# Performance work log

Measured on AMD Instinct MI355X. Metric: run time of the kernel, lower is better.

Reference implementation:

```python
import jax, jax.numpy as jnp
import numpy as np

LMAX = 6
F_IN = 512      # sphere_fdim
F_HID = 8       # f_hidden
N_PTS = 192     # s2 healpix grid points (projector & feature-sphere kernel)
N_SO3GRID = 4000  # SO3Activation grid (resolution=10, ~20x10x20)
N_CONVGRID = 192  # so3_near_identity_grid (8 alpha x 3 beta x 8 gamma)
S2_DIM = (LMAX + 1) ** 2                            # 49
SO3_DIM = sum((2 * l + 1) ** 2 for l in range(LMAX + 1))  # 455
B = 128
C_ENC = 2048
H = W = 7


def setup_inputs() -> dict:
    key = jax.random.key(0)
    ks = jax.random.split(key, 11)
    return {
        "fmap": jax.random.normal(ks[0], (B, C_ENC, H, W), jnp.float32),
        "conv_w": jax.random.normal(ks[1], (F_IN, C_ENC), jnp.float32) / np.sqrt(C_ENC).astype(np.float32),
        "conv_b": jnp.zeros((F_IN,), jnp.float32),
        "proj_w": jax.random.uniform(ks[2], (H, W, N_PTS), jnp.float32) / (H * W),
        "proj_Y": jax.random.normal(ks[3], (N_PTS, S2_DIM), jnp.float32),
        "fs_w": jax.random.normal(ks[4], (F_IN, F_HID, N_PTS), jnp.float32),
        "fs_Y": jax.random.normal(ks[5], (N_PTS, S2_DIM), jnp.float32),
        "act_to": jax.random.normal(ks[6], (SO3_DIM, N_SO3GRID), jnp.float32) / np.sqrt(SO3_DIM).astype(np.float32),
        "act_from": jax.random.normal(ks[7], (N_SO3GRID, SO3_DIM), jnp.float32) / np.float32(N_SO3GRID),
        "so3_w": jax.random.normal(ks[8], (F_HID, 1, N_CONVGRID), jnp.float32),
        "so3_D": jax.random.normal(ks[9], (N_CONVGRID, SO3_DIM), jnp.float32),
    }


def _s2_to_so3_linear(x, psi, f_in):
    # e3nn o3.Linear(s2_irreps -> so3_irreps, internal_weights=False).
    # x: (B, f_in, S2_DIM) with per-l blocks of size 2l+1 (mul=1).
    # psi: (f_in, f_out, S2_DIM). Per l: outer product of input irrep with
    # weight irrep -> (2l+1)x(2l+1) Wigner block; path norm 1/sqrt(f_in*mul_in).
    outs = []
    for l in range(LMAX + 1):
        s, e = l * l, (l + 1) ** 2
        xl = x[:, :, s:e]          # (B, f_in, 2l+1)
        wl = psi[:, :, s:e]        # (f_in, f_out, 2l+1)
        ol = jnp.einsum('bfm,fgu->bgum', xl, wl) / np.sqrt(f_in).astype(np.float32)
        outs.append(ol.reshape(ol.shape[0], ol.shape[1], -1))
    return jnp.concatenate(outs, axis=-1)   # (B, f_out, SO3_DIM)


def _so3_to_so3_linear(x, psi, f_in):
    # e3nn o3.Linear(so3_irreps -> so3_irreps, internal_weights=False).
    # x: (B, f_in, SO3_DIM), per-l block (mul=2l+1, dim=2l+1) flattened [u, m].
    # psi: (f_in, f_out, SO3_DIM), per-l block (u_in, u_out).
    outs = []
    off = 0
    for l in range(LMAX + 1):
        d = 2 * l + 1
        xl = x[:, :, off:off + d * d].reshape(x.shape[0], f_in, d, d)
        wl = psi[:, :, off:off + d * d].reshape(f_in, psi.shape[1], d, d)
        ol = jnp.einsum('bfum,fguv->bgvm', xl, wl) / np.sqrt(f_in * d).astype(np.float32)
        outs.append(ol.reshape(ol.shape[0], ol.shape[1], -1))
        off += d * d
    return jnp.concatenate(outs, axis=-1)


def reference(fmap, conv_w, conv_b, proj_w, proj_Y, fs_w, fs_Y, act_to, act_from, so3_w, so3_D):
    # --- SpatialS2Projector: 1x1 conv, orthographic-grid weighting, S2 FT ---
    x = jnp.einsum('bchw,fc->bfhw', fmap, conv_w) + conv_b[None, :, None, None]
    x = jnp.einsum('bfhw,hwn->bfn', x, proj_w)                   # (B, 512, N_PTS)
    x = jnp.einsum('bfn,ni->bfi', x, proj_Y) / np.sqrt(N_PTS).astype(np.float32)  # (B, 512, 49)
    # --- feature sphere -> external weight for o3.Linear (S2 conv theorem) ---
    psi = jnp.einsum('fgn,ni->fgi', fs_w, fs_Y) / np.sqrt(N_PTS).astype(np.float32)  # (512, 8, 49)
    x = _s2_to_so3_linear(x, psi, F_IN)                          # (B, 8, 455)
    # --- SO3Activation: synthesize signal on SO3 grid, relu, analyze back ---
    g = jax.nn.relu(jnp.einsum('bfi,in->bfn', x, act_to))        # (B, 8, N_SO3GRID)
    x = jnp.einsum('bfn,ni->bfi', g, act_from)                   # (B, 8, 455)
    # --- SO3Convolution over near-identity grid ---
    psi2 = jnp.einsum('fgn,ni->fgi', so3_w, so3_D) / np.sqrt(N_CONVGRID).astype(np.float32)  # (8, 1, 455)
    x = _so3_to_so3_linear(x, psi2, F_HID)                       # (B, 1, 455)
    return x
```

## Files before the change

### kernel.cpp

```cpp
#include <hip/hip_runtime.h>
#include <hip/hip_bf16.h>

#define NB    128
#define CENC  2048
#define FIN   512
#define FHID  8
#define S2D   49
#define SO3D  455
#define HW    49

typedef unsigned short ushort_t;
typedef __bf16 bf16x8 __attribute__((ext_vector_type(8)));
typedef float  f32x4  __attribute__((ext_vector_type(4)));

#define GLD16(gp, lp) __builtin_amdgcn_global_load_lds( \
    (__attribute__((address_space(1))) const unsigned int*)(gp), \
    (__attribute__((address_space(3))) unsigned int*)(lp), 16, 0, 0)

__device__ __forceinline__ int soff(int l) { return l*(4*l*l-1)/3; }

__device__ __forceinline__ ushort_t f2bf(float x) {
  __hip_bfloat16 h = __float2bfloat16(x);
  return *reinterpret_cast<ushort_t*>(&h);
}
__device__ __forceinline__ float bf2f(ushort_t u) {
  __hip_bfloat16 h = *reinterpret_cast<__hip_bfloat16*>(&u);
  return __bfloat162float(h);
}


__device__ __forceinline__ void dev_gemm_nn(float* smem,
    const float* __restrict__ A, const float* __restrict__ B, float* __restrict__ C,
    int M, int N, int K, int lda, int ldb, int ldc, float alpha, int bx, int by)
{
  float* As = smem;
  float* Bs = smem + 32*68;
  const int tid = threadIdx.x;
  const int tx = tid & 15, ty = tid >> 4;
  const int n0 = bx * 64, m0 = by * 64;
  float acc[4][4] = {};
  for (int k0 = 0; k0 < K; k0 += 32) {
    {
      const int kk = tid & 31, mmB = tid >> 5;
      #pragma unroll
      for (int j = 0; j < 8; ++j) {
        const int mm = mmB + 8*j;
        const int m = m0 + mm, k = k0 + kk;
        As[kk*68 + mm] = (m < M && k < K) ? A[(size_t)m*lda + k] : 0.f;
      }
    }
    {
      const int nn = tid & 63, kkB = tid >> 6;
      #pragma unroll
      for (int j = 0; j < 8; ++j) {
        const int kk = kkB + 4*j;
        const int n = n0 + nn, k = k0 + kk;
        Bs[kk*68 + nn] = (n < N && k < K) ? B[(size_t)k*ldb + n] : 0.f;
      }
    }
    __syncthreads();
    #pragma unroll
    for (int kk = 0; kk < 32; ++kk) {
      const float4 a4 = *(const float4*)&As[kk*68 + ty*4];
      const float4 b4 = *(const float4*)&Bs[kk*68 + tx*4];
      const float av[4] = {a4.x,a4.y,a4.z,a4.w};
      const float bv[4] = {b4.x,b4.y,b4.z,b4.w};
      #pragma unroll
      for (int i = 0; i < 4; ++i)
        #pragma unroll
        for (int j = 0; j < 4; ++j)
          acc[i][j] = fmaf(av[i], bv[j], acc[i][j]);
    }
    __syncthreads();
  }
  #pragma unroll
  for (int i = 0; i < 4; ++i) {
    const int m = m0 + ty*4 + i;
    if (m >= M) continue;
    #pragma unroll
    for (int j = 0; j < 4; ++j) {
      const int n = n0 + tx*4 + j;
      if (n >= N) continue;
      C[(size_t)m*ldc + n] = acc[i][j] * alpha;
    }
  }
}

__device__ __forceinline__ void dev_transpose_cvt64(float* smem,
    const float* __restrict__ in, int R, int C,
    ushort_t* __restrict__ out, int Rp, int Cp, int bx, int by)
{
  float (*t)[65] = (float(*)[65])smem;
  const int c0 = bx*64, r0 = by*64;
  const int tid = threadIdx.x;
  const int cl = tid & 63, rlB = tid >> 6;
  #pragma unroll
  for (int p = 0; p < 16; ++p) {
    const int rl = rlB + p*4;
    const int r = r0 + rl, c = c0 + cl;
    t[rl][cl] = (r < R && c < C) ? in[(size_t)r*C + c] : 0.f;
  }
  __syncthreads();
  #pragma unroll
  for (int p = 0; p < 4; ++p) {
    const int c = p*16 + (tid >> 4);
    const int r4 = (tid & 15) * 4;
    unsigned int lo = (unsigned int)f2bf(t[r4+0][c]) | ((unsigned int)f2bf(t[r4+1][c]) << 16);
    unsigned int hi = (unsigned int)f2bf(t[r4+2][c]) | ((unsigned int)f2bf(t[r4+3][c]) << 16);
    *(uint2*)&out[(size_t)(c0 + c)*Rp + r0 + r4] = make_uint2(lo, hi);
  }
}

__device__ __forceinline__ void dev_transpose_fmap(float* smem,
    const float* __restrict__ fmap, ushort_t* __restrict__ out, int cc, int b)
{
  float* Fs = smem;
  const int tid = threadIdx.x;
  const int c0 = cc*128;
  const float* fsrc = fmap + ((size_t)b*CENC + c0)*HW;
  for (int idx = tid; idx < 1568; idx += 256)
    *(float4*)&Fs[idx*4] = *(const float4*)&fsrc[idx*4];
  __syncthreads();
  for (int idx = tid; idx < 1568; idx += 256) {
    const int h = idx >> 5, c4 = (idx & 31) * 4;
    unsigned int lo = (unsigned int)f2bf(Fs[(c4+0)*49 + h]) | ((unsigned int)f2bf(Fs[(c4+1)*49 + h]) << 16);
    unsigned int hi = (unsigned int)f2bf(Fs[(c4+2)*49 + h]) | ((unsigned int)f2bf(Fs[(c4+3)*49 + h]) << 16);
    *(uint2*)&out[(size_t)(b*49 + h)*CENC + c0 + c4] = make_uint2(lo, hi);
  }
}

__device__ __forceinline__ void dev_sumP(float* smem,
    const float* __restrict__ proj_w, const float* __restrict__ proj_Y,
    float* __restrict__ sumP)
{
  float* colsum = smem;
  const int tid = threadIdx.x;
  if (tid < 192) {
    float s = 0.f;
    for (int h = 0; h < 49; ++h) s += proj_w[h*192 + tid];
    colsum[tid] = s;
  }
  __syncthreads();
  if (tid < 64) {
    float s = 0.f;
    if (tid < 49) for (int k = 0; k < 192; ++k) s += colsum[k] * proj_Y[k*49 + tid];
    sumP[tid] = (tid < 49) ? s * 0.07216878364870323f : 0.f;
  }
}

__global__ __launch_bounds__(256) void prep_all(
    const float* __restrict__ fmap, const float* __restrict__ conv_w,
    const float* __restrict__ proj_w, const float* __restrict__ proj_Y,
    const float* __restrict__ fs_w, const float* __restrict__ fs_Y,
    const float* __restrict__ act_to, const float* __restrict__ act_from,
    const float* __restrict__ so3_w, const float* __restrict__ so3_D,
    float* __restrict__ wP, float* __restrict__ wSumP, float* __restrict__ wPsi2,
    float* __restrict__ wPsiP,
    ushort_t* __restrict__ actToT, ushort_t* __restrict__ actFromT,
    ushort_t* __restrict__ cwT, ushort_t* __restrict__ fmapT)
{
  __shared__ float smem[6272];
  const int blk = blockIdx.x;
  const float is192 = 0.07216878364870323f;
  if (blk < 1) {
    dev_gemm_nn(smem, proj_w, proj_Y, wP, 49,49,192, 192,49,49, is192, 0, 0);
  } else if (blk < 9) {
    dev_gemm_nn(smem, so3_w, so3_D, wPsi2, 8,455,192, 192,455,455, is192, blk-1, 0);
  } else if (blk < 73) {
    dev_gemm_nn(smem, fs_w, fs_Y, wPsiP, 4096,49,192, 192,49,128, is192, 0, blk-9);
  } else if (blk < 585) {
    const int t = blk-73;   dev_transpose_cvt64(smem, act_to, 455, 4000, actToT, 512, 4096, t & 63, t >> 6);
  } else if (blk < 1097) {
    const int t = blk-585;  dev_transpose_cvt64(smem, act_from, 4000, 455, actFromT, 4096, 512, t & 7, t >> 3);
  } else if (blk < 1353) {
    const int t = blk-1097; dev_transpose_cvt64(smem, conv_w, 512, 2048, cwT, 512, 2048, t & 31, t >> 5);
  } else if (blk < 3401) {
    const int t = blk-1353; dev_transpose_fmap(smem, fmap, fmapT, t & 15, t >> 4);
  } else {
    dev_sumP(smem, proj_w, proj_Y, wSumP);
  }
}

__global__ __launch_bounds__(256) void psiT_bpsi(
    const float* __restrict__ wPsiP, const float* __restrict__ conv_b,
    ushort_t* __restrict__ psiT, float* __restrict__ bpsi)
{
  const int blk = blockIdx.x, tid = threadIdx.x;
  if (blk < 1024) {
    const int idx = blk*256 + tid;
    const int row = idx >> 9, f = idx & 511;
    const int g = row >> 6, ii = row & 63;
    psiT[idx] = (ii < 49) ? f2bf(wPsiP[(size_t)(f*8 + g)*128 + ii]) : (ushort_t)0;
  } else {
    const int w = tid >> 6, lane = tid & 63;
    const int gi = (blk-1024)*4 + w;
    const int g = gi >> 6, ii = gi & 63;
    float s = 0.f;
    if (ii < 49) {
      #pragma unroll
      for (int s8 = 0; s8 < 8; ++s8) {
        const int f = s8*64 + lane;
        s += conv_b[f] * bf2f(f2bf(wPsiP[(size_t)(f*8 + g)*128 + ii]));
      }
    }
    #pragma unroll
    for (int off = 32; off; off >>= 1) s += __shfl_down(s, off);
    if (lane == 0) bpsi[gi] = s;
  }
}

__global__ __launch_bounds__(256) void gemm4_nt(
    const ushort_t* __restrict__ A, const ushort_t* __restrict__ B, void* __restrict__ Cv,
    int M, int N, int K, int lda, int ldb, int ldc,
    int mode, int kPartLen)
{
  __shared__ ushort_t Alds[64*64];
  __shared__ ushort_t Blds[128*64];
  const int tid = threadIdx.x;
  const int wv = tid >> 6, ln = tid & 63;
  const int col = ln & 15, quad = ln >> 4;
  const int m0 = blockIdx.y * 64, n0 = blockIdx.x * 128;
  int kStart = 0, kEnd = K;
  float*    C  = (float*)Cv;
  ushort_t* Cb = (ushort_t*)Cv;
  if (mode == 2) {
    kStart = blockIdx.z * kPartLen;
    kEnd = min(K, kStart + kPartLen);
    C += (size_t)blockIdx.z * (size_t)M * (size_t)ldc;
  }

  const int rl = ln >> 3;
  const int gsw = (ln & 7) ^ rl;
  const ushort_t* aP[2]; const ushort_t* bP[4];
  ushort_t* aL[2]; ushort_t* bL[4];
  #pragma unroll
  for (int r = 0; r < 2; ++r) {
    const int R = wv*16 + r*8;
    aP[r] = A + (size_t)(m0 + R + rl)*lda + kStart + gsw*8;
    aL[r] = &Alds[R*64];
  }
  #pragma unroll
  for (int r = 0; r < 4; ++r) {
    const int R = wv*32 + r*8;
    bP[r] = B + (size_t)(n0 + R + rl)*ldb + kStart + gsw*8;
    bL[r] = &Blds[R*64];
  }

  f32x4 acc[4][2];
  #pragma unroll
  for (int i = 0; i < 4; ++i)
    #pragma unroll
    for (int j = 0; j < 2; ++j)
      acc[i][j] = (f32x4){0.f,0.f,0.f,0.f};

  for (int k0 = kStart; k0 < kEnd; k0 += 64) {
    #pragma unroll
    for (int r = 0; r < 2; ++r) { GLD16(aP[r], aL[r]); aP[r] += 64; }
    #pragma unroll
    for (int r = 0; r < 4; ++r) { GLD16(bP[r], bL[r]); bP[r] += 64; }
    __syncthreads();
    #pragma unroll
    for (int ks = 0; ks < 2; ++ks) {
      bf16x8 af[4], bfr[2];
      #pragma unroll
      for (int i = 0; i < 4; ++i) {
        const int row = i*16 + col;
        af[i] = *(bf16x8*)&Alds[row*64 + (((ks*4 + quad) ^ (row & 7)) << 3)];
      }
      #pragma unroll
      for (int j = 0; j < 2; ++j) {
        const int row = wv*32 + j*16 + col;
        bfr[j] = *(bf16x8*)&Blds[row*64 + (((ks*4 + quad) ^ (row & 7)) << 3)];
      }
      #pragma unroll
      for (int i = 0; i < 4; ++i)
        #pragma unroll
        for (int j = 0; j < 2; ++j)
          acc[i][j] = __builtin_amdgcn_mfma_f32_16x16x32_bf16(af[i], bfr[j], acc[i][j], 0, 0, 0);
    }
    __syncthreads();
  }

  #pragma unroll
  for (int i = 0; i < 4; ++i) {
    const int mBase = m0 + i*16 + quad*4;
    #pragma unroll
    for (int j = 0; j < 2; ++j) {
      const int n = n0 + wv*32 + j*16 + col;
      if (mode == 1) {
        #pragma unroll
        for (int r = 0; r < 4; ++r)
          Cb[(size_t)(mBase+r)*ldc + n] = f2bf(fmaxf(acc[i][j][r], 0.f));
      } else if (mode == 3) {
        #pragma unroll
        for (int r = 0; r < 4; ++r)
          Cb[(size_t)(mBase+r)*ldc + n] = f2bf(acc[i][j][r]);
      } else {
        #pragma unroll
        for (int r = 0; r < 4; ++r)
          C[(size_t)(mBase+r)*ldc + n] = acc[i][j][r];
      }
    }
  }
}

__global__ __launch_bounds__(256) void gather_y(
    const float* __restrict__ T, const float* __restrict__ P,
    const float* __restrict__ sumP, const float* __restrict__ bpsi,
    ushort_t* __restrict__ y)
{
  __shared__ float Tg[49*64];
  __shared__ float Pl[49*49];
  __shared__ float sPl[49];
  __shared__ float bps[64];
  const int tid = threadIdx.x;
  const int g = blockIdx.x & 7, b = blockIdx.x >> 3;
  for (int idx = tid; idx < 49*64; idx += 256) {
    const int h = idx >> 6, c = idx & 63;
    Tg[idx] = T[(size_t)(b*49 + h)*512 + g*64 + c];
  }
  for (int idx = tid; idx < 2401; idx += 256) Pl[idx] = P[idx];
  if (tid < 49) sPl[tid] = sumP[tid];
  if (tid < 64) bps[tid] = bpsi[g*64 + tid];
  __syncthreads();
  #pragma unroll
  for (int rr = 0; rr < 2; ++rr) {
    const int j = tid + rr*256;
    float v = 0.f;
    if (j < SO3D) {
      int l;
      if (j < 1) l = 0; else if (j < 10) l = 1; else if (j < 35) l = 2;
      else if (j < 84) l = 3; else if (j < 165) l = 4; else if (j < 286) l = 5; else l = 6;
      const int so = soff(l), d = 2*l+1;
      const int r = j - so;
      const int u = r / d, m = r - u*d;
      const int i = l*l + m, colT = l*l + u;
      float acc = 0.f;
      #pragma unroll 7
      for (int h = 0; h < 49; ++h)
        acc = fmaf(Pl[h*49 + i], Tg[h*64 + colT], acc);
      v = (acc + sPl[i]*bps[colT]) * 0.044194173824159216f;
    }
    y[(size_t)(b*8+g)*512 + j] = f2bf(v);
  }
}

__global__ __launch_bounds__(512) void so3_final(
    const float* __restrict__ zpart, const float* __restrict__ psi2,
    float* __restrict__ out)
{
  __shared__ float Zs[8*SO3D];
  __shared__ float P2s[8*SO3D];
  const int b = blockIdx.x, tid = threadIdx.x;
  for (int idx = tid; idx < 8*SO3D; idx += 512) {
    const int f = idx / SO3D, i = idx - f*SO3D;
    float s = 0.f;
    #pragma unroll
    for (int p = 0; p < 8; ++p)
      s += zpart[((size_t)p*1024 + (size_t)b*FHID + f)*512 + i];
    Zs[idx] = s;
    P2s[idx] = psi2[idx];
  }
  __syncthreads();
  if (tid < SO3D) {
    const int i = tid;
    int l;
    if (i < 1) l = 0; else if (i < 10) l = 1; else if (i < 35) l = 2;
    else if (i < 84) l = 3; else if (i < 165) l = 4; else if (i < 286) l = 5; else l = 6;
    const int so = soff(l), d = 2*l+1;
    const int r = i - so;
    const int v = r / d, m = r - v*d;
    float acc = 0.f;
    for (int f = 0; f < 8; ++f)
      for (int u = 0; u < d; ++u)
        acc = fmaf(Zs[f*SO3D + so + u*d + m], P2s[f*SO3D + so + u*d + v], acc);
    const float scale = rsqrtf(8.0f * (float)d);
    out[(size_t)b*SO3D + i] = acc * scale;
  }
}

extern "C" void kernel_launch(void* const* d_in, const int* in_sizes, int n_in,
                              void* d_out, int out_size, void* d_ws, size_t ws_size,
                              hipStream_t stream) {
  const float* fmap    = (const float*)d_in[0];
  const float* conv_w  = (const float*)d_in[1];
  const float* conv_b  = (const float*)d_in[2];
  const float* proj_w  = (const float*)d_in[3];
  const float* proj_Y  = (const float*)d_in[4];
  const float* fs_w    = (const float*)d_in[5];
  const float* fs_Y    = (const float*)d_in[6];
  const float* act_to  = (const float*)d_in[7];
  const float* act_from= (const float*)d_in[8];
  const float* so3_w   = (const float*)d_in[9];
  const float* so3_D   = (const float*)d_in[10];
  float* out           = (float*)d_out;

  char* wsb = (char*)d_ws;
  float*    wP       = (float*)(wsb + 0);
  float*    wSumP    = (float*)(wsb + 9728);
  float*    wPsi2    = (float*)(wsb + 9984);
  ushort_t* actToT   = (ushort_t*)(wsb + 24576);
  ushort_t* actFromT = (ushort_t*)(wsb + 4218880);
  ushort_t* yPad     = (ushort_t*)(wsb + 8413184);
  ushort_t* psiT     = (ushort_t*)(wsb + 9461760);
  float*    bpsi     = (float*)(wsb + 9986048);
  ushort_t* W2T      = (ushort_t*)(wsb + 9988096);
  ushort_t* fmapT    = (ushort_t*)(wsb + 12085248);
  float*    wPsiP    = (float*)(wsb + 37775360);
  ushort_t* cwT      = (ushort_t*)(wsb + 39872512);
  float*    Tbuf     = (float*)(wsb + 41969664);
  ushort_t* gBuf     = (ushort_t*)(wsb + 12085248);
  float*    zPart    = (float*)(wsb + 20473856);

  prep_all<<<dim3(3402), 256, 0, stream>>>(
      fmap, conv_w, proj_w, proj_Y, fs_w, fs_Y, act_to, act_from, so3_w, so3_D,
      wP, wSumP, wPsi2, wPsiP, actToT, actFromT, cwT, fmapT);
  psiT_bpsi<<<dim3(1152), 256, 0, stream>>>(wPsiP, conv_b, psiT, bpsi);
  gemm4_nt<<<dim3(16,8), 256, 0, stream>>>(psiT, cwT, W2T,
      512, 2048, 512, 512, 512, 2048, 3, 0);
  gemm4_nt<<<dim3(4,98), 256, 0, stream>>>(fmapT, W2T, Tbuf,
      6272, 512, 2048, 2048, 2048, 512, 0, 0);
  gather_y<<<dim3(1024), 256, 0, stream>>>(Tbuf, wP, wSumP, bpsi, yPad);
  gemm4_nt<<<dim3(32,16), 256, 0, stream>>>(yPad, actToT, gBuf,
      1024, 4096, 512, 512, 512, 4096, 1, 0);
  gemm4_nt<<<dim3(4,16,8), 256, 0, stream>>>(gBuf, actFromT, zPart,
      1024, 512, 4096, 4096, 4096, 512, 2, 512);
  so3_final<<<dim3(128), 512, 0, stream>>>(zPart, wPsi2, out);
}
```

Before: 234.4 us.

## Fuse psi transpose and bias reduction into prep and W2T GEMM, enlarge GEMM tiles

The fs_w×fs_Y GEMM in prep now writes the transposed bf16 psiT directly, and the separate psiT_bpsi kernel is removed. The conv-bias projection (bpsi) is computed inside a dedicated W2T GEMM from the staged A tiles. The remaining bf16 GEMMs move from 64x128 to 128x128 tiles with a 2x2 wave layout, giving more MFMA work per LDS load and fewer blocks. The fmap transpose uses smaller 64-channel chunks to cut shared memory per block. Costs are higher register use and fewer blocks for the large GEMMs, which may lower occupancy. psiT is also now written with a strided, uncoalesced pattern.

```diff
diff --git a/kernel.cpp b/kernel.cpp
--- a/kernel.cpp
+++ b/kernel.cpp
@@ -31,7 +31,8 @@
 
 __device__ __forceinline__ void dev_gemm_nn(float* smem,
     const float* __restrict__ A, const float* __restrict__ B, float* __restrict__ C,
-    int M, int N, int K, int lda, int ldb, int ldc, float alpha, int bx, int by)
+    int M, int N, int K, int lda, int ldb, int ldc, float alpha, int bx, int by,
+    int cmode, ushort_t* __restrict__ psiTout)
 {
   float* As = smem;
   float* Bs = smem + 32*68;
@@ -73,6 +74,19 @@
     }
     __syncthreads();
   }
+  if (cmode == 1) {
+    #pragma unroll
+    for (int i = 0; i < 4; ++i) {
+      const int m = m0 + ty*4 + i;
+      const int f = m >> 3, g = m & 7;
+      #pragma unroll
+      for (int j = 0; j < 4; ++j) {
+        const int n = tx*4 + j;
+        psiTout[(size_t)(g*64 + n)*512 + f] = (n < 49) ? f2bf(acc[i][j]*alpha) : (ushort_t)0;
+      }
+    }
+    return;
+  }
   #pragma unroll
   for (int i = 0; i < 4; ++i) {
     const int m = m0 + ty*4 + i;
@@ -116,13 +130,13 @@
 {
   float* Fs = smem;
   const int tid = threadIdx.x;
-  const int c0 = cc*128;
+  const int c0 = cc*64;
   const float* fsrc = fmap + ((size_t)b*CENC + c0)*HW;
-  for (int idx = tid; idx < 1568; idx += 256)
+  for (int idx = tid; idx < 784; idx += 256)
     *(float4*)&Fs[idx*4] = *(const float4*)&fsrc[idx*4];
   __syncthreads();
-  for (int idx = tid; idx < 1568; idx += 256) {
-    const int h = idx >> 5, c4 = (idx & 31) * 4;
+  for (int idx = tid; idx < 784; idx += 256) {
+    const int h = idx >> 4, c4 = (idx & 15) * 4;
     unsigned int lo = (unsigned int)f2bf(Fs[(c4+0)*49 + h]) | ((unsigned int)f2bf(Fs[(c4+1)*49 + h]) << 16);
     unsigned int hi = (unsigned int)f2bf(Fs[(c4+2)*49 + h]) | ((unsigned int)f2bf(Fs[(c4+3)*49 + h]) << 16);
     *(uint2*)&out[(size_t)(b*49 + h)*CENC + c0 + c4] = make_uint2(lo, hi);
@@ -155,71 +169,142 @@
     const float* __restrict__ act_to, const float* __restrict__ act_from,
     const float* __restrict__ so3_w, const float* __restrict__ so3_D,
     float* __restrict__ wP, float* __restrict__ wSumP, float* __restrict__ wPsi2,
-    float* __restrict__ wPsiP,
+    ushort_t* __restrict__ psiT,
     ushort_t* __restrict__ actToT, ushort_t* __restrict__ actFromT,
     ushort_t* __restrict__ cwT, ushort_t* __restrict__ fmapT)
 {
-  __shared__ float smem[6272];
+  __shared__ float smem[4352];
   const int blk = blockIdx.x;
   const float is192 = 0.07216878364870323f;
   if (blk < 1) {
-    dev_gemm_nn(smem, proj_w, proj_Y, wP, 49,49,192, 192,49,49, is192, 0, 0);
+    dev_gemm_nn(smem, proj_w, proj_Y, wP, 49,49,192, 192,49,49, is192, 0, 0, 0, nullptr);
   } else if (blk < 9) {
-    dev_gemm_nn(smem, so3_w, so3_D, wPsi2, 8,455,192, 192,455,455, is192, blk-1, 0);
+    dev_gemm_nn(smem, so3_w, so3_D, wPsi2, 8,455,192, 192,455,455, is192, blk-1, 0, 0, nullptr);
   } else if (blk < 73) {
-    dev_gemm_nn(smem, fs_w, fs_Y, wPsiP, 4096,49,192, 192,49,128, is192, 0, blk-9);
+    dev_gemm_nn(smem, fs_w, fs_Y, nullptr, 4096,49,192, 192,49,0, is192, 0, blk-9, 1, psiT);
   } else if (blk < 585) {
     const int t = blk-73;   dev_transpose_cvt64(smem, act_to, 455, 4000, actToT, 512, 4096, t & 63, t >> 6);
   } else if (blk < 1097) {
     const int t = blk-585;  dev_transpose_cvt64(smem, act_from, 4000, 455, actFromT, 4096, 512, t & 7, t >> 3);
   } else if (blk < 1353) {
     const int t = blk-1097; dev_transpose_cvt64(smem, conv_w, 512, 2048, cwT, 512, 2048, t & 31, t >> 5);
-  } else if (blk < 3401) {
-    const int t = blk-1353; dev_transpose_fmap(smem, fmap, fmapT, t & 15, t >> 4);
+  } else if (blk < 5449) {
+    const int t = blk-1353; dev_transpose_fmap(smem, fmap, fmapT, t & 31, t >> 5);
   } else {
     dev_sumP(smem, proj_w, proj_Y, wSumP);
   }
 }
 
-__global__ __launch_bounds__(256) void psiT_bpsi(
-    const float* __restrict__ wPsiP, const float* __restrict__ conv_b,
-    ushort_t* __restrict__ psiT, float* __restrict__ bpsi)
-{
-  const int blk = blockIdx.x, tid = threadIdx.x;
-  if (blk < 1024) {
-    const int idx = blk*256 + tid;
-    const int row = idx >> 9, f = idx & 511;
-    const int g = row >> 6, ii = row & 63;
-    psiT[idx] = (ii < 49) ? f2bf(wPsiP[(size_t)(f*8 + g)*128 + ii]) : (ushort_t)0;
-  } else {
-    const int w = tid >> 6, lane = tid & 63;
-    const int gi = (blk-1024)*4 + w;
-    const int g = gi >> 6, ii = gi & 63;
-    float s = 0.f;
-    if (ii < 49) {
-      #pragma unroll
-      for (int s8 = 0; s8 < 8; ++s8) {
-        const int f = s8*64 + lane;
-        s += conv_b[f] * bf2f(f2bf(wPsiP[(size_t)(f*8 + g)*128 + ii]));
-      }
-    }
-    #pragma unroll
-    for (int off = 32; off; off >>= 1) s += __shfl_down(s, off);
-    if (lane == 0) bpsi[gi] = s;
-  }
-}
-
-__global__ __launch_bounds__(256) void gemm4_nt(
+__global__ __launch_bounds__(256) void gemm_w2t(
+    const ushort_t* __restrict__ A, const ushort_t* __restrict__ B,
+    const float* __restrict__ conv_b,
+    ushort_t* __restrict__ Cb, float* __restrict__ bpsi)
+{
+  __shared__ ushort_t Alds[64*64];
+  __shared__ ushort_t Blds[128*64];
+  __shared__ float bred[256];
+  const int tid = threadIdx.x;
+  const int wv = tid >> 6, ln = tid & 63;
+  const int col = ln & 15, quad = ln >> 4;
+  const int m0 = blockIdx.y * 64, n0 = blockIdx.x * 128;
+  const int lda = 512, ldb = 512, ldc = 2048, K = 512;
+  const bool doB = (blockIdx.x == 0);
+  const int br = tid & 63, bp = tid >> 6;
+
+  const int rl = ln >> 3;
+  const int gsw = (ln & 7) ^ rl;
+  const ushort_t* aP[2]; const ushort_t* bP[4];
+  ushort_t* aL[2]; ushort_t* bL[4];
+  #pragma unroll
+  for (int r = 0; r < 2; ++r) {
+    const int R = wv*16 + r*8;
+    aP[r] = A + (size_t)(m0 + R + rl)*lda + gsw*8;
+    aL[r] = &Alds[R*64];
+  }
+  #pragma unroll
+  for (int r = 0; r < 4; ++r) {
+    const int R = wv*32 + r*8;
+    bP[r] = B + (size_t)(n0 + R + rl)*ldb + gsw*8;
+    bL[r] = &Blds[R*64];
+  }
+
+  f32x4 acc[4][2];
+  #pragma unroll
+  for (int i = 0; i < 4; ++i)
+    #pragma unroll
+    for (int j = 0; j < 2; ++j)
+      acc[i][j] = (f32x4){0.f,0.f,0.f,0.f};
+  float bacc = 0.f;
+
+  for (int k0 = 0; k0 < K; k0 += 64) {
+    #pragma unroll
+    for (int r = 0; r < 2; ++r) { GLD16(aP[r], aL[r]); aP[r] += 64; }
+    #pragma unroll
+    for (int r = 0; r < 4; ++r) { GLD16(bP[r], bL[r]); bP[r] += 64; }
+    __syncthreads();
+    #pragma unroll
+    for (int ks = 0; ks < 2; ++ks) {
+      bf16x8 af[4], bfr[2];
+      #pragma unroll
+      for (int i = 0; i < 4; ++i) {
+        const int row = i*16 + col;
+        af[i] = *(bf16x8*)&Alds[row*64 + (((ks*4 + quad) ^ (row & 7)) << 3)];
+      }
+      #pragma unroll
+      for (int j = 0; j < 2; ++j) {
+        const int row = wv*32 + j*16 + col;
+        bfr[j] = *(bf16x8*)&Blds[row*64 + (((ks*4 + quad) ^ (row & 7)) << 3)];
+      }
+      #pragma unroll
+      for (int i = 0; i < 4; ++i)
+        #pragma unroll
+        for (int j = 0; j < 2; ++j)
+          acc[i][j] = __builtin_amdgcn_mfma_f32_16x16x32_bf16(af[i], bfr[j], acc[i][j], 0, 0, 0);
+    }
+    if (doB) {
+      #pragma unroll
+      for (int qq = 0; qq < 2; ++qq) {
+        const int q = bp*2 + qq;
+        const int lo = (q ^ (br & 7)) << 3;
+        #pragma unroll
+        for (int e = 0; e < 8; ++e)
+          bacc = fmaf(conv_b[k0 + q*8 + e], bf2f(Alds[br*64 + lo + e]), bacc);
+      }
+    }
+    __syncthreads();
+  }
+
+  #pragma unroll
+  for (int i = 0; i < 4; ++i) {
+    const int mBase = m0 + i*16 + quad*4;
+    #pragma unroll
+    for (int j = 0; j < 2; ++j) {
+      const int n = n0 + wv*32 + j*16 + col;
+      #pragma unroll
+      for (int r = 0; r < 4; ++r)
+        Cb[(size_t)(mBase+r)*ldc + n] = f2bf(acc[i][j][r]);
+    }
+  }
+  if (doB) {
+    bred[bp*64 + br] = bacc;
+    __syncthreads();
+    if (tid < 64)
+      bpsi[m0 + tid] = bred[tid] + bred[64+tid] + bred[128+tid] + bred[192+tid];
+  }
+}
+
+__global__ __launch_bounds__(256) void gemm8_nt(
     const ushort_t* __restrict__ A, const ushort_t* __restrict__ B, void* __restrict__ Cv,
     int M, int N, int K, int lda, int ldb, int ldc,
     int mode, int kPartLen)
 {
-  __shared__ ushort_t Alds[64*64];
+  __shared__ ushort_t Alds[128*64];
   __shared__ ushort_t Blds[128*64];
   const int tid = threadIdx.x;
   const int wv = tid >> 6, ln = tid & 63;
   const int col = ln & 15, quad = ln >> 4;
-  const int m0 = blockIdx.y * 64, n0 = blockIdx.x * 128;
+  const int wr = wv >> 1, wc = wv & 1;
+  const int m0 = blockIdx.y * 128, n0 = blockIdx.x * 128;
   int kStart = 0, kEnd = K;
   float*    C  = (float*)Cv;
   ushort_t* Cb = (ushort_t*)Cv;
@@ -231,51 +316,47 @@
 
   const int rl = ln >> 3;
   const int gsw = (ln & 7) ^ rl;
-  const ushort_t* aP[2]; const ushort_t* bP[4];
-  ushort_t* aL[2]; ushort_t* bL[4];
-  #pragma unroll
-  for (int r = 0; r < 2; ++r) {
-    const int R = wv*16 + r*8;
+  const ushort_t* aP[4]; const ushort_t* bP[4];
+  ushort_t* aL[4]; ushort_t* bL[4];
+  #pragma unroll
+  for (int r = 0; r < 4; ++r) {
+    const int R = r*32 + wv*8;
     aP[r] = A + (size_t)(m0 + R + rl)*lda + kStart + gsw*8;
     aL[r] = &Alds[R*64];
-  }
-  #pragma unroll
-  for (int r = 0; r < 4; ++r) {
-    const int R = wv*32 + r*8;
     bP[r] = B + (size_t)(n0 + R + rl)*ldb + kStart + gsw*8;
     bL[r] = &Blds[R*64];
   }
 
-  f32x4 acc[4][2];
+  f32x4 acc[4][4];
   #pragma unroll
   for (int i = 0; i < 4; ++i)
     #pragma unroll
-    for (int j = 0; j < 2; ++j)
+    for (int j = 0; j < 4; ++j)
       acc[i][j] = (f32x4){0.f,0.f,0.f,0.f};
 
   for (int k0 = kStart; k0 < kEnd; k0 += 64) {
     #pragma unroll
-    for (int r = 0; r < 2; ++r) { GLD16(aP[r], aL[r]); aP[r] += 64; }
+    for (int r = 0; r < 4; ++r) { GLD16(aP[r], aL[r]); aP[r] += 64; }
     #pragma unroll
     for (int r = 0; r < 4; ++r) { GLD16(bP[r], bL[r]); bP[r] += 64; }
     __syncthreads();
     #pragma unroll
     for (int ks = 0; ks < 2; ++ks) {
-      bf16x8 af[4], bfr[2];
+      bf16x8 af[4], bfr[4];
       #pragma unroll
       for (int i = 0; i < 4; ++i) {
-        const int row = i*16 + col;
+        const int row = wr*64 + i*16 + col;
         af[i] = *(bf16x8*)&Alds[row*64 + (((ks*4 + quad) ^ (row & 7)) << 3)];
       }
       #pragma unroll
-      for (int j = 0; j < 2; ++j) {
-        const int row = wv*32 + j*16 + col;
+      for (int j = 0; j < 4; ++j) {
+        const int row = wc*64 + j*16 + col;
         bfr[j] = *(bf16x8*)&Blds[row*64 + (((ks*4 + quad) ^ (row & 7)) << 3)];
       }
       #pragma unroll
       for (int i = 0; i < 4; ++i)
         #pragma unroll
-        for (int j = 0; j < 2; ++j)
+        for (int j = 0; j < 4; ++j)
           acc[i][j] = __builtin_amdgcn_mfma_f32_16x16x32_bf16(af[i], bfr[j], acc[i][j], 0, 0, 0);
     }
     __syncthreads();
@@ -283,19 +364,15 @@
 
   #pragma unroll
   for (int i = 0; i < 4; ++i) {
-    const int mBase = m0 + i*16 + quad*4;
-    #pragma unroll
-    for (int j = 0; j < 2; ++j) {
-      const int n = n0 + wv*32 + j*16 + col;
+    const int mBase = m0 + wr*64 + i*16 + quad*4;
+    #pragma unroll
+    for (int j = 0; j < 4; ++j) {
+      const int n = n0 + wc*64 + j*16 + col;
       if (mode == 1) {
         #pragma unroll
         for (int r = 0; r < 4; ++r)
           Cb[(size_t)(mBase+r)*ldc + n] = f2bf(fmaxf(acc[i][j][r], 0.f));
-      } else if (mode == 3) {
-        #pragma unroll
-        for (int r = 0; r < 4; ++r)
-          Cb[(size_t)(mBase+r)*ldc + n] = f2bf(acc[i][j][r]);
-      } else {
+      } else if (mode == 2 || mode == 0) {
         #pragma unroll
         for (int r = 0; r < 4; ++r)
           C[(size_t)(mBase+r)*ldc + n] = acc[i][j][r];
@@ -406,24 +483,21 @@
   float*    bpsi     = (float*)(wsb + 9986048);
   ushort_t* W2T      = (ushort_t*)(wsb + 9988096);
   ushort_t* fmapT    = (ushort_t*)(wsb + 12085248);
-  float*    wPsiP    = (float*)(wsb + 37775360);
   ushort_t* cwT      = (ushort_t*)(wsb + 39872512);
   float*    Tbuf     = (float*)(wsb + 41969664);
   ushort_t* gBuf     = (ushort_t*)(wsb + 12085248);
   float*    zPart    = (float*)(wsb + 20473856);
 
-  prep_all<<<dim3(3402), 256, 0, stream>>>(
+  prep_all<<<dim3(5450), 256, 0, stream>>>(
       fmap, conv_w, proj_w, proj_Y, fs_w, fs_Y, act_to, act_from, so3_w, so3_D,
-      wP, wSumP, wPsi2, wPsiP, actToT, actFromT, cwT, fmapT);
-  psiT_bpsi<<<dim3(1152), 256, 0, stream>>>(wPsiP, conv_b, psiT, bpsi);
-  gemm4_nt<<<dim3(16,8), 256, 0, stream>>>(psiT, cwT, W2T,
-      512, 2048, 512, 512, 512, 2048, 3, 0);
-  gemm4_nt<<<dim3(4,98), 256, 0, stream>>>(fmapT, W2T, Tbuf,
+      wP, wSumP, wPsi2, psiT, actToT, actFromT, cwT, fmapT);
+  gemm_w2t<<<dim3(16,8), 256, 0, stream>>>(psiT, cwT, conv_b, W2T, bpsi);
+  gemm8_nt<<<dim3(4,49), 256, 0, stream>>>(fmapT, W2T, Tbuf,
       6272, 512, 2048, 2048, 2048, 512, 0, 0);
   gather_y<<<dim3(1024), 256, 0, stream>>>(Tbuf, wP, wSumP, bpsi, yPad);
-  gemm4_nt<<<dim3(32,16), 256, 0, stream>>>(yPad, actToT, gBuf,
+  gemm8_nt<<<dim3(32,8), 256, 0, stream>>>(yPad, actToT, gBuf,
       1024, 4096, 512, 512, 512, 4096, 1, 0);
-  gemm4_nt<<<dim3(4,16,8), 256, 0, stream>>>(gBuf, actFromT, zPart,
+  gemm8_nt<<<dim3(4,8,8), 256, 0, stream>>>(gBuf, actFromT, zPart,
       1024, 512, 4096, 4096, 4096, 512, 2, 512);
   so3_final<<<dim3(128), 512, 0, stream>>>(zPart, wPsi2, out);
 }
```

Measured after the change: 242.8 us. +3.6%, slower.
